# Performance work log

Hardware: AMD Instinct MI355X
Metric: run time of the kernel (lower is better)

The kernel has to match this reference:

```python
import jax, jax.numpy as jnp
import numpy as np

B = 4096
NQ = 4  # qubits -> 16-dim state vector


def _make_ops(seed, n_ops):
    # Deterministic stand-in for tq.RandomLayer: random RX/RY/RZ/CRX gates.
    rng = np.random.default_rng(seed)
    ops = []
    for _ in range(n_ops):
        kind = int(rng.integers(0, 4))
        if kind == 3:  # CRX on two distinct wires
            w = rng.choice(NQ, size=2, replace=False)
            ops.append((3, int(w[0]), int(w[1])))
        else:
            ops.append((kind, int(rng.integers(0, NQ)), 0))
    return ops

ENC_OPS = _make_ops(1, 8)    # QuantumPatchEncoder.random_layer (n_ops=8)
QFC_OPS = _make_ops(2, 50)   # QuantumFullyConnectedLayer.random_layer (n_ops=50)

_H = np.array([[1, 1], [1, -1]], np.complex64) * np.complex64(1.0 / np.sqrt(2.0))
_SX = np.array([[1 + 1j, 1 - 1j], [1 - 1j, 1 + 1j]], np.complex64) * np.complex64(0.5)
_CNOT = np.array([[1, 0, 0, 0], [0, 1, 0, 0], [0, 0, 0, 1], [0, 0, 1, 0]], np.complex64)


def _rx(t):
    c = jnp.cos(t / 2) + 0j
    s = -1j * jnp.sin(t / 2)
    return jnp.stack([jnp.stack([c, s], -1), jnp.stack([s, c], -1)], -2)


def _ry(t):
    c = jnp.cos(t / 2) + 0j
    s = jnp.sin(t / 2) + 0j
    return jnp.stack([jnp.stack([c, -s], -1), jnp.stack([s, c], -1)], -2)


def _rz(t):
    e0 = jnp.exp(-1j * t / 2)
    e1 = jnp.exp(1j * t / 2)
    z = jnp.zeros_like(e0)
    return jnp.stack([jnp.stack([e0, z], -1), jnp.stack([z, e1], -1)], -2)


def _crx(t):
    return jnp.eye(4, dtype=jnp.complex64).at[2:, 2:].set(_rx(t))


def _apply1(state, U, w):
    # state: (B, 2,2,2,2); U: (2,2) or per-sample (B,2,2)
    state = jnp.moveaxis(state, w + 1, -1)
    if U.ndim == 3:
        state = jnp.einsum('b...i,bji->b...j', state, U)
    else:
        state = jnp.einsum('...i,ji->...j', state, U)
    return jnp.moveaxis(state, -1, w + 1)


def _apply2(state, U, w0, w1):
    state = jnp.moveaxis(state, (w0 + 1, w1 + 1), (-2, -1))
    shp = state.shape
    state = state.reshape(shp[:-2] + (4,)) @ U.T
    return jnp.moveaxis(state.reshape(shp), (-2, -1), (w0 + 1, w1 + 1))


def _random_layer(state, ops, params):
    for i, (kind, w0, w1) in enumerate(ops):
        t = params[i]
        if kind == 0:
            state = _apply1(state, _rx(t), w0)
        elif kind == 1:
            state = _apply1(state, _ry(t), w0)
        elif kind == 2:
            state = _apply1(state, _rz(t), w0)
        else:
            state = _apply2(state, _crx(t), w0, w1)
    return state


def _measure_z(state):
    # <Z> on each wire from |amp|^2 marginals
    probs = state.real ** 2 + state.imag ** 2
    exps = []
    for w in range(NQ):
        axes = tuple(a for a in range(1, NQ + 1) if a != w + 1)
        m = probs.sum(axes)  # (B, 2)
        exps.append(m[:, 0] - m[:, 1])
    return jnp.stack(exps, 1)


def _conv(x, W, b):
    y = jax.lax.conv_general_dilated(x, W, (1, 1), 'SAME',
                                     dimension_numbers=('NCHW', 'OIHW', 'NCHW'))
    return y + b[None, :, None, None]


def _pool(x):
    return jax.lax.reduce_window(x, -jnp.inf, jax.lax.max,
                                 (1, 1, 2, 2), (1, 1, 2, 2), 'VALID')


def setup_inputs() -> dict:
    key = jax.random.key(0)
    ks = jax.random.split(key, 8)
    f = lambda k, shp, fan: jax.random.normal(k, shp, jnp.float32) / np.float32(np.sqrt(fan))
    two_pi = float(2 * np.pi)
    return {
        'x': jax.random.uniform(ks[0], (B, 1, 32, 32), jnp.float32),
        'conv1_w': f(ks[1], (8, 1, 3, 3), 9),
        'conv1_b': jnp.zeros((8,), jnp.float32),
        'conv2_w': f(ks[2], (16, 8, 3, 3), 72),
        'conv2_b': jnp.zeros((16,), jnp.float32),
        'enc_params': jax.random.uniform(ks[3], (8,), jnp.float32, 0.0, two_pi),
        'qfc_rand_params': jax.random.uniform(ks[4], (50,), jnp.float32, 0.0, two_pi),
        'qfc_params': jax.random.uniform(ks[5], (4,), jnp.float32, 0.0, two_pi),
        'bn_gamma': jnp.ones((4,), jnp.float32),
        'bn_beta': jnp.zeros((4,), jnp.float32),
        'fc_w': f(ks[6], (10, 68), 68),
        'fc_b': jnp.zeros((10,), jnp.float32),
    }


def reference(x, conv1_w, conv1_b, conv2_w, conv2_b, enc_params, qfc_rand_params,
              qfc_params, bn_gamma, bn_beta, fc_w, fc_b):
    # CNN feature extractor
    h = _pool(jax.nn.relu(_conv(x, conv1_w, conv1_b)))
    h = _pool(jax.nn.relu(_conv(h, conv2_w, conv2_b)))  # (B, 16, 8, 8)
    b = h.shape[0]
    pm = h.mean(1)  # channel-mean, (B, 8, 8)
    # 2x2 patches, row-major within patch, scanning r then c -> (B, 16, 4)
    patches = pm.reshape(b, 4, 2, 4, 2).transpose(0, 1, 3, 2, 4).reshape(b, 16, 4)

    # Encoder: fresh |0000> per patch (GeneralEncoder resets state); batch all
    # B*16 patch circuits together instead of looping.
    data = patches.reshape(b * 16, 4)
    state = jnp.zeros((b * 16, 16), jnp.complex64).at[:, 0].set(1.0)
    state = state.reshape(b * 16, 2, 2, 2, 2)
    for w in range(NQ):
        state = _apply1(state, _ry(data[:, w]), w)
    state = _random_layer(state, ENC_OPS, enc_params)
    qfeat = _measure_z(state).reshape(b, 64)  # (B, 16*4)

    # QFC operates on the state left by the LAST patch (as in the original)
    s = state.reshape(b, 16, 2, 2, 2, 2)[:, 15]
    s = _random_layer(s, QFC_OPS, qfc_rand_params)
    s = _apply1(s, _rx(qfc_params[0]), 0)
    s = _apply1(s, _ry(qfc_params[1]), 1)
    s = _apply1(s, _rz(qfc_params[2]), 3)
    s = _apply2(s, _crx(qfc_params[3]), 0, 2)
    s = _apply1(s, jnp.asarray(_H), 3)
    s = _apply1(s, jnp.asarray(_SX), 2)
    s = _apply2(s, jnp.asarray(_CNOT), 3, 0)
    q = _measure_z(s)  # (B, 4)

    # BatchNorm1d(4), training-mode (batch stats, biased var)
    mu = q.mean(0)
    var = q.var(0)
    q = (q - mu) / jnp.sqrt(var + 1e-5) * bn_gamma + bn_beta

    feats = jnp.concatenate([qfeat, q], 1)  # (B, 68)
    logits = feats @ fc_w.T + fc_b
    return jax.nn.log_softmax(logits, -1)
```

## Files before the change

kernel.cpp:

```cpp
#include <hip/hip_runtime.h>
#include <cstdint>

namespace crng {

typedef unsigned __int128 u128;

struct PCG {
    u128 state, inc;
    bool has32;
    uint32_t buf32;
};

constexpr u128 PCG_MULT = (((u128)2549297995355413924ULL) << 64) | (u128)4865540595714422341ULL;

constexpr uint64_t pcg_next64(PCG& g) {
    g.state = g.state * PCG_MULT + g.inc;
    uint64_t hi = (uint64_t)(g.state >> 64), lo = (uint64_t)g.state;
    unsigned rot = (unsigned)(g.state >> 122) & 63u;
    uint64_t v = hi ^ lo;
    return (v >> rot) | (v << ((64u - rot) & 63u));
}

constexpr uint32_t pcg_next32(PCG& g) {
    if (g.has32) { g.has32 = false; return g.buf32; }
    uint64_t n = pcg_next64(g);
    g.has32 = true;
    g.buf32 = (uint32_t)(n >> 32);
    return (uint32_t)n;
}

constexpr uint32_t hashmix(uint32_t& hc, uint32_t v) {
    v ^= hc; hc *= 0x931e8875u; v *= hc; v ^= v >> 16; return v;
}
constexpr uint32_t mixf(uint32_t x, uint32_t y) {
    uint32_t r = 0xca01f9ddu * x - 0x4973f715u * y;
    r ^= r >> 16;
    return r;
}

constexpr PCG seed_pcg(uint32_t entropy) {
    uint32_t pool[4] = {0, 0, 0, 0};
    uint32_t hc = 0x43b0d7e5u;
    pool[0] = hashmix(hc, entropy);
    for (int i = 1; i < 4; ++i) pool[i] = hashmix(hc, 0u);
    for (int s = 0; s < 4; ++s)
        for (int d = 0; d < 4; ++d)
            if (s != d) pool[d] = mixf(pool[d], hashmix(hc, pool[s]));

    uint32_t hb = 0x8b51f9ddu;
    uint32_t w[8] = {0, 0, 0, 0, 0, 0, 0, 0};
    for (int i = 0; i < 8; ++i) {
        uint32_t dv = pool[i & 3];
        dv ^= hb; hb *= 0x58f38dedu; dv *= hb; dv ^= dv >> 16;
        w[i] = dv;
    }
    uint64_t w64[4] = {0, 0, 0, 0};
    for (int i = 0; i < 4; ++i)
        w64[i] = (uint64_t)w[2 * i] | ((uint64_t)w[2 * i + 1] << 32);

    u128 initstate = (((u128)w64[0]) << 64) | (u128)w64[1];
    u128 initseq   = (((u128)w64[2]) << 64) | (u128)w64[3];
    PCG g = {};
    g.state = 0;
    g.inc = (initseq << 1) | (u128)1;
    g.state = g.state * PCG_MULT + g.inc;
    g.state += initstate;
    g.state = g.state * PCG_MULT + g.inc;
    g.has32 = false;
    g.buf32 = 0;
    return g;
}

constexpr uint32_t lemire32(PCG& g, uint32_t rng) {
    uint64_t rng_excl = (uint64_t)rng + 1;
    uint64_t m = (uint64_t)pcg_next32(g) * rng_excl;
    uint32_t leftover = (uint32_t)m;
    if (leftover < (uint32_t)rng_excl) {
        uint32_t threshold = (uint32_t)((uint64_t)(0xFFFFFFFFu - rng) % rng_excl);
        while (leftover < threshold) {
            m = (uint64_t)pcg_next32(g) * rng_excl;
            leftover = (uint32_t)m;
        }
    }
    return (uint32_t)(m >> 32);
}

struct Ops {
    int enc[8];
    int qfc[50];
};

constexpr void fill_ops(PCG& g, int n, int* out) {
    for (int i = 0; i < n; ++i) {
        uint32_t kind = lemire32(g, 3);
        uint32_t w0 = 0, w1 = 0;
        if (kind == 3) {
            uint32_t v2 = lemire32(g, 2);
            uint32_t v3 = lemire32(g, 3);
            uint32_t a0 = v2;
            uint32_t a1 = (v3 == v2) ? 3u : v3;
            uint32_t j = lemire32(g, 1);
            if (j == 0) { uint32_t t = a0; a0 = a1; a1 = t; }
            w0 = a0; w1 = a1;
        } else {
            w0 = lemire32(g, 3);
        }
        out[i] = (int)((kind << 4) | (w0 << 2) | w1);
    }
}

constexpr Ops make_ops_ct() {
    Ops o = {};
    PCG g1 = seed_pcg(1u);
    fill_ops(g1, 8, o.enc);
    PCG g2 = seed_pcg(2u);
    fill_ops(g2, 50, o.qfc);
    return o;
}

}

constexpr crng::Ops kOps = crng::make_ops_ct();

typedef _Float16 half8 __attribute__((ext_vector_type(8)));
typedef float float4v __attribute__((ext_vector_type(4)));

#define XS_STRIDE 24
#define XS_PLANE  (34 * XS_STRIDE)
#define XS_TOT    (2 * XS_PLANE)
#define H1F_ROW   (18 * 8)

__global__ __launch_bounds__(256, 4) void cnn_kernel(
    const float* __restrict__ x, const float* __restrict__ w1,
    const float* __restrict__ b1, const float* __restrict__ w2,
    const float* __restrict__ b2, float* __restrict__ pm,
    float* __restrict__ stats)
{
    __shared__ float xs[XS_TOT];
    __shared__ __align__(16) _Float16 h1f[18 * H1F_ROW];
    __shared__ __align__(16) _Float16 Ahalf[9 * 16 * 8];
    __shared__ float w1s[72], b1s[8], b2s[16];

    const int tid = threadIdx.x;
    const int b = blockIdx.x;
    const float* xb = x + (size_t)b * 1024;

    for (int k = tid; k < XS_TOT; k += 256) xs[k] = 0.f;
    for (int k = tid; k < 18 * H1F_ROW; k += 256) h1f[k] = (_Float16)0.f;
    for (int e = tid; e < 1152; e += 256) {
        int uv = e >> 7, m = (e >> 3) & 15, ci = e & 7;
        Ahalf[e] = (_Float16)w2[m * 72 + ci * 9 + uv];
    }
    if (tid < 72) w1s[tid] = w1[tid];
    if (tid < 8) b1s[tid] = b1[tid];
    if (tid < 16) b2s[tid] = b2[tid];
    if (b == 0 && tid < 8) stats[tid] = 0.f;
    __syncthreads();

    for (int k = tid; k < 1024; k += 256) {
        int r = k >> 5, c = k & 31;
        int p = c & 1;
        int q = p ? ((c + 1) >> 1) : (c >> 1);
        xs[p * XS_PLANE + (r + 1) * XS_STRIDE + q] = xb[k];
    }
    __syncthreads();

    {
        const int i = tid >> 4, j = tid & 15;
        float patch[4][4];
#pragma unroll
        for (int u = 0; u < 4; ++u) {
            int r = 2 * i + u;
            const float* ev = &xs[r * XS_STRIDE + j];
            const float* od = &xs[XS_PLANE + r * XS_STRIDE + j];
            patch[u][0] = od[0];
            patch[u][1] = ev[0];
            patch[u][2] = od[1];
            patch[u][3] = ev[1];
        }
        half8 hv;
#pragma unroll
        for (int c = 0; c < 8; ++c) {
            float m = -3.4e38f;
#pragma unroll
            for (int di = 0; di < 2; ++di)
#pragma unroll
                for (int dj = 0; dj < 2; ++dj) {
                    float acc = b1s[c];
#pragma unroll
                    for (int u = 0; u < 3; ++u)
#pragma unroll
                        for (int v = 0; v < 3; ++v)
                            acc += w1s[c * 9 + u * 3 + v] * patch[di + u][dj + v];
                    m = fmaxf(m, acc);
                }
            hv[c] = (_Float16)fmaxf(m, 0.f);
        }
        *(half8*)&h1f[(i + 1) * H1F_ROW + (j + 1) * 8] = hv;
    }
    __syncthreads();

    {
        const int w = tid >> 6;
        const int lane = tid & 63;
        const int pj = lane & 15;
        const int quad = lane >> 4;

        half8 afrag[9];
#pragma unroll
        for (int uv = 0; uv < 9; ++uv) {
            half8 a = {};
            if (quad == 0) a = *(const half8*)&Ahalf[(uv * 16 + pj) * 8];
            afrag[uv] = a;
        }

        float4v acc[4];
#pragma unroll
        for (int tl = 0; tl < 4; ++tl) {
            float4v c;
#pragma unroll
            for (int r = 0; r < 4; ++r) c[r] = b2s[4 * quad + r];
            acc[tl] = c;
        }

#pragma unroll
        for (int tl = 0; tl < 4; ++tl) {
            const int t = 4 * w + tl;
#pragma unroll
            for (int u = 0; u < 3; ++u) {
#pragma unroll
                for (int v = 0; v < 3; ++v) {
                    half8 bf = *(const half8*)&h1f[(t + u) * H1F_ROW + (pj + v) * 8];
                    acc[tl] = __builtin_amdgcn_mfma_f32_16x16x32_f16(
                        afrag[u * 3 + v], bf, acc[tl], 0, 0, 0);
                }
            }
        }

#pragma unroll
        for (int p = 0; p < 2; ++p) {
            float4v m1;
#pragma unroll
            for (int r = 0; r < 4; ++r)
                m1[r] = fmaxf(acc[2 * p][r], acc[2 * p + 1][r]);
            float s = 0.f;
#pragma unroll
            for (int r = 0; r < 4; ++r) {
                float o = __shfl_xor((float)m1[r], 1, 64);
                float mv = fmaxf(fmaxf(m1[r], o), 0.f);
                s += mv;
            }
            s += __shfl_xor(s, 16, 64);
            s += __shfl_xor(s, 32, 64);
            if (quad == 0 && !(pj & 1)) {
                const int i2 = 2 * w + p, j2 = pj >> 1;
                pm[(size_t)b * 64 + i2 * 8 + j2] = s * (1.f / 16.f);
            }
        }
    }
}

template<int KIND, int W0, int W1>
__device__ __forceinline__ void gate_ct(float (&ur)[16], float (&ui)[16],
                                        float ch, float sh)
{
    constexpr bool CTRL = (KIND == 3 || KIND == 6);
    constexpr int STT = CTRL ? (8 >> W1) : (8 >> W0);
    constexpr int STC = CTRL ? (8 >> W0) : 0;
#pragma unroll
    for (int k0 = 0; k0 < 16; ++k0) {
        if (k0 & STT) continue;
        if (STC != 0 && !(k0 & STC)) continue;
        const int k1 = k0 | STT;
        float x0r = ur[k0], x0i = ui[k0], x1r = ur[k1], x1i = ui[k1];
        if constexpr (KIND == 0 || KIND == 3) {
            ur[k0] = ch * x0r + sh * x1i;  ui[k0] = ch * x0i - sh * x1r;
            ur[k1] = sh * x0i + ch * x1r;  ui[k1] = -sh * x0r + ch * x1i;
        } else if constexpr (KIND == 1) {
            ur[k0] = ch * x0r - sh * x1r;  ui[k0] = ch * x0i - sh * x1i;
            ur[k1] = sh * x0r + ch * x1r;  ui[k1] = sh * x0i + ch * x1i;
        } else if constexpr (KIND == 2) {
            ur[k0] = ch * x0r + sh * x0i;  ui[k0] = ch * x0i - sh * x0r;
            ur[k1] = ch * x1r - sh * x1i;  ui[k1] = ch * x1i + sh * x1r;
        } else if constexpr (KIND == 4) {
            constexpr float RH = 0.70710678118654752f;
            ur[k0] = RH * (x0r + x1r);  ui[k0] = RH * (x0i + x1i);
            ur[k1] = RH * (x0r - x1r);  ui[k1] = RH * (x0i - x1i);
        } else if constexpr (KIND == 5) {
            ur[k0] = 0.5f * (x0r + x1r) - 0.5f * x0i + 0.5f * x1i;
            ui[k0] = 0.5f * (x0i + x1i) + 0.5f * x0r - 0.5f * x1r;
            ur[k1] = 0.5f * (x0r + x1r) + 0.5f * x0i - 0.5f * x1i;
            ui[k1] = 0.5f * (x0i + x1i) - 0.5f * x0r + 0.5f * x1r;
        } else {
            ur[k0] = x1r; ui[k0] = x1i;
            ur[k1] = x0r; ui[k1] = x0i;
        }
    }
}

template<int I>
__device__ __forceinline__ void run_enc(float (&ur)[16], float (&ui)[16],
                                        const float* ch, const float* sh)
{
    if constexpr (I < 8) {
        constexpr int op = kOps.enc[I];
        gate_ct<(op >> 4) & 7, (op >> 2) & 3, op & 3>(ur, ui, ch[I], sh[I]);
        run_enc<I + 1>(ur, ui, ch, sh);
    }
}

template<int I>
__device__ __forceinline__ void run_qfc(float (&ur)[16], float (&ui)[16],
                                        const float* ch, const float* sh)
{
    if constexpr (I < 50) {
        constexpr int op = kOps.qfc[I];
        gate_ct<(op >> 4) & 7, (op >> 2) & 3, op & 3>(ur, ui, ch[I], sh[I]);
        run_qfc<I + 1>(ur, ui, ch, sh);
    }
}

__global__ __launch_bounds__(256) void quantum_kernel(
    const float* __restrict__ pm, const float* __restrict__ encp,
    const float* __restrict__ qfcr, const float* __restrict__ qfcp,
    float* __restrict__ qfeat, float* __restrict__ qraw,
    float* __restrict__ stats, int Bv)
{
    __shared__ float chs[62], shs[62];
    __shared__ float rstat[128];

    const int tid = threadIdx.x;
    if (tid < 62) {
        float t = (tid < 8) ? encp[tid] : (tid < 58) ? qfcr[tid - 8] : qfcp[tid - 58];
        chs[tid] = cosf(0.5f * t);
        shs[tid] = sinf(0.5f * t);
    }
    __syncthreads();

    const int gid = blockIdx.x * 256 + tid;
    const int b = gid >> 4, p = gid & 15;
    float qq[4] = {0.f, 0.f, 0.f, 0.f};
    bool last = false;

    if (b < Bv) {
        const int pr = p >> 2, pc = p & 3;
        const float* pmb = pm + (size_t)b * 64;
        float d0 = pmb[(2 * pr) * 8 + 2 * pc];
        float d1 = pmb[(2 * pr) * 8 + 2 * pc + 1];
        float d2 = pmb[(2 * pr + 1) * 8 + 2 * pc];
        float d3 = pmb[(2 * pr + 1) * 8 + 2 * pc + 1];
        float f0c = cosf(0.5f * d0), f0s = sinf(0.5f * d0);
        float f1c = cosf(0.5f * d1), f1s = sinf(0.5f * d1);
        float f2c = cosf(0.5f * d2), f2s = sinf(0.5f * d2);
        float f3c = cosf(0.5f * d3), f3s = sinf(0.5f * d3);

        float ur[16], ui[16];
#pragma unroll
        for (int k = 0; k < 16; ++k) {
            float v = ((k & 8) ? f0s : f0c);
            v *= ((k & 4) ? f1s : f1c);
            v *= ((k & 2) ? f2s : f2c);
            v *= ((k & 1) ? f3s : f3c);
            ur[k] = v;
            ui[k] = 0.f;
        }
        run_enc<0>(ur, ui, chs, shs);

        float qv[4] = {0.f, 0.f, 0.f, 0.f};
#pragma unroll
        for (int k = 0; k < 16; ++k) {
            float pk = ur[k] * ur[k] + ui[k] * ui[k];
            qv[0] += (k & 8) ? -pk : pk;
            qv[1] += (k & 4) ? -pk : pk;
            qv[2] += (k & 2) ? -pk : pk;
            qv[3] += (k & 1) ? -pk : pk;
        }
        *(float4*)(qfeat + (size_t)b * 64 + p * 4) = make_float4(qv[0], qv[1], qv[2], qv[3]);

        if (p == 15) {
            last = true;
            run_qfc<0>(ur, ui, chs + 8, shs + 8);
            gate_ct<0, 0, 0>(ur, ui, chs[58], shs[58]);
            gate_ct<1, 1, 0>(ur, ui, chs[59], shs[59]);
            gate_ct<2, 3, 0>(ur, ui, chs[60], shs[60]);
            gate_ct<3, 0, 2>(ur, ui, chs[61], shs[61]);
            gate_ct<4, 3, 0>(ur, ui, 0.f, 0.f);
            gate_ct<5, 2, 0>(ur, ui, 0.f, 0.f);
            gate_ct<6, 3, 0>(ur, ui, 0.f, 0.f);
#pragma unroll
            for (int k = 0; k < 16; ++k) {
                float pk = ur[k] * ur[k] + ui[k] * ui[k];
                qq[0] += (k & 8) ? -pk : pk;
                qq[1] += (k & 4) ? -pk : pk;
                qq[2] += (k & 2) ? -pk : pk;
                qq[3] += (k & 1) ? -pk : pk;
            }
            *(float4*)(qraw + (size_t)b * 4) = make_float4(qq[0], qq[1], qq[2], qq[3]);
        }
    }

    for (int k = tid; k < 128; k += 256) rstat[k] = 0.f;
    __syncthreads();
    const int m = tid >> 4;
    if (last) {
#pragma unroll
        for (int w = 0; w < 4; ++w) {
            rstat[w * 16 + m] = qq[w];
            rstat[64 + w * 16 + m] = qq[w] * qq[w];
        }
    }
    __syncthreads();
    if (tid < 8) {
        float s = 0.f;
#pragma unroll
        for (int k = 0; k < 16; ++k) s += rstat[tid * 16 + k];
        atomicAdd(&stats[tid], s);
    }
}

__global__ __launch_bounds__(256) void head_kernel(
    const float* __restrict__ qfeat, const float* __restrict__ qraw,
    const float* __restrict__ stats, const float* __restrict__ gam,
    const float* __restrict__ bet, const float* __restrict__ fcw,
    const float* __restrict__ fcb, float* __restrict__ out, int Bv)
{
    __shared__ float Wf[680];
    __shared__ float bf[10], st[8], ga[4], be[4];
    const int tid = threadIdx.x;
    for (int k = tid; k < 680; k += 256) Wf[k] = fcw[k];
    if (tid < 10) bf[tid] = fcb[tid];
    if (tid < 8) st[tid] = stats[tid];
    if (tid < 4) { ga[tid] = gam[tid]; be[tid] = bet[tid]; }
    __syncthreads();

    const int b = blockIdx.x * 256 + tid;
    if (b >= Bv) return;

    const float invB = 1.f / (float)Bv;

    float logit[10];
#pragma unroll
    for (int k = 0; k < 10; ++k) logit[k] = bf[k];

    const float* qf = qfeat + (size_t)b * 64;
    for (int j = 0; j < 64; ++j) {
        float v = qf[j];
#pragma unroll
        for (int k = 0; k < 10; ++k) logit[k] += v * Wf[k * 68 + j];
    }
    float4 qr = *(const float4*)(qraw + (size_t)b * 4);
    float qn[4] = {qr.x, qr.y, qr.z, qr.w};
#pragma unroll
    for (int w = 0; w < 4; ++w) {
        float mu = st[w] * invB;
        float var = st[4 + w] * invB - mu * mu;
        float v = (qn[w] - mu) / sqrtf(var + 1e-5f) * ga[w] + be[w];
#pragma unroll
        for (int k = 0; k < 10; ++k) logit[k] += v * Wf[k * 68 + 64 + w];
    }

    float m = logit[0];
#pragma unroll
    for (int k = 1; k < 10; ++k) m = fmaxf(m, logit[k]);
    float sum = 0.f;
#pragma unroll
    for (int k = 0; k < 10; ++k) sum += expf(logit[k] - m);
    float lse = logf(sum);
#pragma unroll
    for (int k = 0; k < 10; ++k) out[(size_t)b * 10 + k] = logit[k] - m - lse;
}

extern "C" void kernel_launch(void* const* d_in, const int* in_sizes, int n_in,
                              void* d_out, int out_size, void* d_ws, size_t ws_size,
                              hipStream_t stream)
{
    const float* x    = (const float*)d_in[0];
    const float* w1   = (const float*)d_in[1];
    const float* b1   = (const float*)d_in[2];
    const float* w2   = (const float*)d_in[3];
    const float* b2   = (const float*)d_in[4];
    const float* encp = (const float*)d_in[5];
    const float* qfcr = (const float*)d_in[6];
    const float* qfcp = (const float*)d_in[7];
    const float* gam  = (const float*)d_in[8];
    const float* bet  = (const float*)d_in[9];
    const float* fcw  = (const float*)d_in[10];
    const float* fcb  = (const float*)d_in[11];
    float* out = (float*)d_out;

    const int Bv = in_sizes[0] / 1024;

    float* pm    = (float*)d_ws;
    float* qfeat = pm + (size_t)Bv * 64;
    float* qraw  = qfeat + (size_t)Bv * 64;
    float* stats = qraw + (size_t)Bv * 4;

    cnn_kernel<<<Bv, 256, 0, stream>>>(x, w1, b1, w2, b2, pm, stats);
    quantum_kernel<<<(Bv * 16 + 255) / 256, 256, 0, stream>>>(
        pm, encp, qfcr, qfcp, qfeat, qraw, stats, Bv);
    head_kernel<<<(Bv + 255) / 256, 256, 0, stream>>>(qfeat, qraw, stats, gam, bet,
                                                      fcw, fcb, out, Bv);
}
```

Measured before the change: 140.4 us.

## Fuse CNN with encoder and QFC with head using grid barrier

Runs the patch encoder inside the CNN kernel on pooled features kept in LDS, so the pm buffer and the separate quantum kernel go away. The QFC circuit, BatchNorm statistics and the FC/log-softmax head now share one tail kernel, with a software grid barrier on an atomic counter between the stats reduction and the normalisation. Also vectorises the input load and qfeat reads and replaces the LDS stat reduction with wave shuffles. This removes one launch and some global round trips. The spin barrier assumes all 16 tail blocks are co-resident, and the encoder now runs on only 16 of 256 threads per block.

Result: faster. 129.6 us (-7.7%).

```diff
diff --git a/kernel.cpp b/kernel.cpp
--- a/kernel.cpp
+++ b/kernel.cpp
@@ -129,136 +129,6 @@
 #define XS_PLANE  (34 * XS_STRIDE)
 #define XS_TOT    (2 * XS_PLANE)
 #define H1F_ROW   (18 * 8)
-
-__global__ __launch_bounds__(256, 4) void cnn_kernel(
-    const float* __restrict__ x, const float* __restrict__ w1,
-    const float* __restrict__ b1, const float* __restrict__ w2,
-    const float* __restrict__ b2, float* __restrict__ pm,
-    float* __restrict__ stats)
-{
-    __shared__ float xs[XS_TOT];
-    __shared__ __align__(16) _Float16 h1f[18 * H1F_ROW];
-    __shared__ __align__(16) _Float16 Ahalf[9 * 16 * 8];
-    __shared__ float w1s[72], b1s[8], b2s[16];
-
-    const int tid = threadIdx.x;
-    const int b = blockIdx.x;
-    const float* xb = x + (size_t)b * 1024;
-
-    for (int k = tid; k < XS_TOT; k += 256) xs[k] = 0.f;
-    for (int k = tid; k < 18 * H1F_ROW; k += 256) h1f[k] = (_Float16)0.f;
-    for (int e = tid; e < 1152; e += 256) {
-        int uv = e >> 7, m = (e >> 3) & 15, ci = e & 7;
-        Ahalf[e] = (_Float16)w2[m * 72 + ci * 9 + uv];
-    }
-    if (tid < 72) w1s[tid] = w1[tid];
-    if (tid < 8) b1s[tid] = b1[tid];
-    if (tid < 16) b2s[tid] = b2[tid];
-    if (b == 0 && tid < 8) stats[tid] = 0.f;
-    __syncthreads();
-
-    for (int k = tid; k < 1024; k += 256) {
-        int r = k >> 5, c = k & 31;
-        int p = c & 1;
-        int q = p ? ((c + 1) >> 1) : (c >> 1);
-        xs[p * XS_PLANE + (r + 1) * XS_STRIDE + q] = xb[k];
-    }
-    __syncthreads();
-
-    {
-        const int i = tid >> 4, j = tid & 15;
-        float patch[4][4];
-#pragma unroll
-        for (int u = 0; u < 4; ++u) {
-            int r = 2 * i + u;
-            const float* ev = &xs[r * XS_STRIDE + j];
-            const float* od = &xs[XS_PLANE + r * XS_STRIDE + j];
-            patch[u][0] = od[0];
-            patch[u][1] = ev[0];
-            patch[u][2] = od[1];
-            patch[u][3] = ev[1];
-        }
-        half8 hv;
-#pragma unroll
-        for (int c = 0; c < 8; ++c) {
-            float m = -3.4e38f;
-#pragma unroll
-            for (int di = 0; di < 2; ++di)
-#pragma unroll
-                for (int dj = 0; dj < 2; ++dj) {
-                    float acc = b1s[c];
-#pragma unroll
-                    for (int u = 0; u < 3; ++u)
-#pragma unroll
-                        for (int v = 0; v < 3; ++v)
-                            acc += w1s[c * 9 + u * 3 + v] * patch[di + u][dj + v];
-                    m = fmaxf(m, acc);
-                }
-            hv[c] = (_Float16)fmaxf(m, 0.f);
-        }
-        *(half8*)&h1f[(i + 1) * H1F_ROW + (j + 1) * 8] = hv;
-    }
-    __syncthreads();
-
-    {
-        const int w = tid >> 6;
-        const int lane = tid & 63;
-        const int pj = lane & 15;
-        const int quad = lane >> 4;
-
-        half8 afrag[9];
-#pragma unroll
-        for (int uv = 0; uv < 9; ++uv) {
-            half8 a = {};
-            if (quad == 0) a = *(const half8*)&Ahalf[(uv * 16 + pj) * 8];
-            afrag[uv] = a;
-        }
-
-        float4v acc[4];
-#pragma unroll
-        for (int tl = 0; tl < 4; ++tl) {
-            float4v c;
-#pragma unroll
-            for (int r = 0; r < 4; ++r) c[r] = b2s[4 * quad + r];
-            acc[tl] = c;
-        }
-
-#pragma unroll
-        for (int tl = 0; tl < 4; ++tl) {
-            const int t = 4 * w + tl;
-#pragma unroll
-            for (int u = 0; u < 3; ++u) {
-#pragma unroll
-                for (int v = 0; v < 3; ++v) {
-                    half8 bf = *(const half8*)&h1f[(t + u) * H1F_ROW + (pj + v) * 8];
-                    acc[tl] = __builtin_amdgcn_mfma_f32_16x16x32_f16(
-                        afrag[u * 3 + v], bf, acc[tl], 0, 0, 0);
-                }
-            }
-        }
-
-#pragma unroll
-        for (int p = 0; p < 2; ++p) {
-            float4v m1;
-#pragma unroll
-            for (int r = 0; r < 4; ++r)
-                m1[r] = fmaxf(acc[2 * p][r], acc[2 * p + 1][r]);
-            float s = 0.f;
-#pragma unroll
-            for (int r = 0; r < 4; ++r) {
-                float o = __shfl_xor((float)m1[r], 1, 64);
-                float mv = fmaxf(fmaxf(m1[r], o), 0.f);
-                s += mv;
-            }
-            s += __shfl_xor(s, 16, 64);
-            s += __shfl_xor(s, 32, 64);
-            if (quad == 0 && !(pj & 1)) {
-                const int i2 = 2 * w + p, j2 = pj >> 1;
-                pm[(size_t)b * 64 + i2 * 8 + j2] = s * (1.f / 16.f);
-            }
-        }
-    }
-}
 
 template<int KIND, int W0, int W1>
 __device__ __forceinline__ void gate_ct(float (&ur)[16], float (&ui)[16],
@@ -320,35 +190,155 @@
     }
 }
 
-__global__ __launch_bounds__(256) void quantum_kernel(
-    const float* __restrict__ pm, const float* __restrict__ encp,
-    const float* __restrict__ qfcr, const float* __restrict__ qfcp,
-    float* __restrict__ qfeat, float* __restrict__ qraw,
-    float* __restrict__ stats, int Bv)
+__global__ __launch_bounds__(256, 4) void cnn_enc_kernel(
+    const float* __restrict__ x, const float* __restrict__ w1,
+    const float* __restrict__ b1, const float* __restrict__ w2,
+    const float* __restrict__ b2, const float* __restrict__ encp,
+    float* __restrict__ qfeat, float* __restrict__ sstate,
+    float* __restrict__ stats, int* __restrict__ bar)
 {
-    __shared__ float chs[62], shs[62];
-    __shared__ float rstat[128];
+    __shared__ float xs[XS_TOT];
+    __shared__ __align__(16) _Float16 h1f[18 * H1F_ROW];
+    __shared__ __align__(16) _Float16 Ahalf[9 * 16 * 8];
+    __shared__ float w1s[72], b1s[8], b2s[16];
+    __shared__ float pm_lds[64];
+    __shared__ float chsE[8], shsE[8];
 
     const int tid = threadIdx.x;
-    if (tid < 62) {
-        float t = (tid < 8) ? encp[tid] : (tid < 58) ? qfcr[tid - 8] : qfcp[tid - 58];
-        chs[tid] = cosf(0.5f * t);
-        shs[tid] = sinf(0.5f * t);
-    }
-    __syncthreads();
-
-    const int gid = blockIdx.x * 256 + tid;
-    const int b = gid >> 4, p = gid & 15;
-    float qq[4] = {0.f, 0.f, 0.f, 0.f};
-    bool last = false;
-
-    if (b < Bv) {
-        const int pr = p >> 2, pc = p & 3;
-        const float* pmb = pm + (size_t)b * 64;
-        float d0 = pmb[(2 * pr) * 8 + 2 * pc];
-        float d1 = pmb[(2 * pr) * 8 + 2 * pc + 1];
-        float d2 = pmb[(2 * pr + 1) * 8 + 2 * pc];
-        float d3 = pmb[(2 * pr + 1) * 8 + 2 * pc + 1];
+    const int b = blockIdx.x;
+    const float* xb = x + (size_t)b * 1024;
+
+    for (int k = tid; k < XS_TOT; k += 256) xs[k] = 0.f;
+    for (int k = tid; k < 18 * H1F_ROW; k += 256) h1f[k] = (_Float16)0.f;
+    for (int e = tid; e < 1152; e += 256) {
+        int uv = e >> 7, m = (e >> 3) & 15, ci = e & 7;
+        Ahalf[e] = (_Float16)w2[m * 72 + ci * 9 + uv];
+    }
+    if (tid < 72) w1s[tid] = w1[tid];
+    if (tid < 8) b1s[tid] = b1[tid];
+    if (tid < 16) b2s[tid] = b2[tid];
+    if (tid < 8) {
+        float t = encp[tid];
+        chsE[tid] = cosf(0.5f * t);
+        shsE[tid] = sinf(0.5f * t);
+    }
+    if (b == 0 && tid < 8) stats[tid] = 0.f;
+    if (b == 0 && tid == 8) *bar = 0;
+    __syncthreads();
+
+    {
+        const int r = tid >> 3, m = tid & 7;
+        float4 v = *(const float4*)(xb + (size_t)tid * 4);
+        float* d0p = &xs[(r + 1) * XS_STRIDE + 2 * m];
+        float* d1p = &xs[XS_PLANE + (r + 1) * XS_STRIDE + 2 * m];
+        d0p[0] = v.x;
+        d1p[1] = v.y;
+        d0p[1] = v.z;
+        d1p[2] = v.w;
+    }
+    __syncthreads();
+
+    {
+        const int i = tid >> 4, j = tid & 15;
+        float patch[4][4];
+#pragma unroll
+        for (int u = 0; u < 4; ++u) {
+            int r = 2 * i + u;
+            const float* ev = &xs[r * XS_STRIDE + j];
+            const float* od = &xs[XS_PLANE + r * XS_STRIDE + j];
+            patch[u][0] = od[0];
+            patch[u][1] = ev[0];
+            patch[u][2] = od[1];
+            patch[u][3] = ev[1];
+        }
+        half8 hv;
+#pragma unroll
+        for (int c = 0; c < 8; ++c) {
+            float m = -3.4e38f;
+#pragma unroll
+            for (int di = 0; di < 2; ++di)
+#pragma unroll
+                for (int dj = 0; dj < 2; ++dj) {
+                    float acc = b1s[c];
+#pragma unroll
+                    for (int u = 0; u < 3; ++u)
+#pragma unroll
+                        for (int v = 0; v < 3; ++v)
+                            acc += w1s[c * 9 + u * 3 + v] * patch[di + u][dj + v];
+                    m = fmaxf(m, acc);
+                }
+            hv[c] = (_Float16)fmaxf(m, 0.f);
+        }
+        *(half8*)&h1f[(i + 1) * H1F_ROW + (j + 1) * 8] = hv;
+    }
+    __syncthreads();
+
+    {
+        const int w = tid >> 6;
+        const int lane = tid & 63;
+        const int pj = lane & 15;
+        const int quad = lane >> 4;
+
+        half8 afrag[9];
+#pragma unroll
+        for (int uv = 0; uv < 9; ++uv) {
+            half8 a = {};
+            if (quad == 0) a = *(const half8*)&Ahalf[(uv * 16 + pj) * 8];
+            afrag[uv] = a;
+        }
+
+        float4v acc[4];
+#pragma unroll
+        for (int tl = 0; tl < 4; ++tl) {
+            float4v c;
+#pragma unroll
+            for (int r = 0; r < 4; ++r) c[r] = b2s[4 * quad + r];
+            acc[tl] = c;
+        }
+
+#pragma unroll
+        for (int tl = 0; tl < 4; ++tl) {
+            const int t = 4 * w + tl;
+#pragma unroll
+            for (int u = 0; u < 3; ++u) {
+#pragma unroll
+                for (int v = 0; v < 3; ++v) {
+                    half8 bf = *(const half8*)&h1f[(t + u) * H1F_ROW + (pj + v) * 8];
+                    acc[tl] = __builtin_amdgcn_mfma_f32_16x16x32_f16(
+                        afrag[u * 3 + v], bf, acc[tl], 0, 0, 0);
+                }
+            }
+        }
+
+#pragma unroll
+        for (int p = 0; p < 2; ++p) {
+            float4v m1;
+#pragma unroll
+            for (int r = 0; r < 4; ++r)
+                m1[r] = fmaxf(acc[2 * p][r], acc[2 * p + 1][r]);
+            float s = 0.f;
+#pragma unroll
+            for (int r = 0; r < 4; ++r) {
+                float o = __shfl_xor((float)m1[r], 1, 64);
+                float mv = fmaxf(fmaxf(m1[r], o), 0.f);
+                s += mv;
+            }
+            s += __shfl_xor(s, 16, 64);
+            s += __shfl_xor(s, 32, 64);
+            if (quad == 0 && !(pj & 1)) {
+                const int i2 = 2 * w + p, j2 = pj >> 1;
+                pm_lds[i2 * 8 + j2] = s * (1.f / 16.f);
+            }
+        }
+    }
+    __syncthreads();
+
+    if (tid < 16) {
+        const int p = tid, pr = p >> 2, pc = p & 3;
+        float d0 = pm_lds[(2 * pr) * 8 + 2 * pc];
+        float d1 = pm_lds[(2 * pr) * 8 + 2 * pc + 1];
+        float d2 = pm_lds[(2 * pr + 1) * 8 + 2 * pc];
+        float d3 = pm_lds[(2 * pr + 1) * 8 + 2 * pc + 1];
         float f0c = cosf(0.5f * d0), f0s = sinf(0.5f * d0);
         float f1c = cosf(0.5f * d1), f1s = sinf(0.5f * d1);
         float f2c = cosf(0.5f * d2), f2s = sinf(0.5f * d2);
@@ -364,7 +354,7 @@
             ur[k] = v;
             ui[k] = 0.f;
         }
-        run_enc<0>(ur, ui, chs, shs);
+        run_enc<0>(ur, ui, chsE, shsE);
 
         float qv[4] = {0.f, 0.f, 0.f, 0.f};
 #pragma unroll
@@ -375,86 +365,135 @@
             qv[2] += (k & 2) ? -pk : pk;
             qv[3] += (k & 1) ? -pk : pk;
         }
-        *(float4*)(qfeat + (size_t)b * 64 + p * 4) = make_float4(qv[0], qv[1], qv[2], qv[3]);
+        *(float4*)(qfeat + (size_t)b * 64 + p * 4) =
+            make_float4(qv[0], qv[1], qv[2], qv[3]);
 
         if (p == 15) {
-            last = true;
-            run_qfc<0>(ur, ui, chs + 8, shs + 8);
-            gate_ct<0, 0, 0>(ur, ui, chs[58], shs[58]);
-            gate_ct<1, 1, 0>(ur, ui, chs[59], shs[59]);
-            gate_ct<2, 3, 0>(ur, ui, chs[60], shs[60]);
-            gate_ct<3, 0, 2>(ur, ui, chs[61], shs[61]);
-            gate_ct<4, 3, 0>(ur, ui, 0.f, 0.f);
-            gate_ct<5, 2, 0>(ur, ui, 0.f, 0.f);
-            gate_ct<6, 3, 0>(ur, ui, 0.f, 0.f);
-#pragma unroll
-            for (int k = 0; k < 16; ++k) {
-                float pk = ur[k] * ur[k] + ui[k] * ui[k];
-                qq[0] += (k & 8) ? -pk : pk;
-                qq[1] += (k & 4) ? -pk : pk;
-                qq[2] += (k & 2) ? -pk : pk;
-                qq[3] += (k & 1) ? -pk : pk;
-            }
-            *(float4*)(qraw + (size_t)b * 4) = make_float4(qq[0], qq[1], qq[2], qq[3]);
-        }
-    }
-
-    for (int k = tid; k < 128; k += 256) rstat[k] = 0.f;
-    __syncthreads();
-    const int m = tid >> 4;
-    if (last) {
-#pragma unroll
-        for (int w = 0; w < 4; ++w) {
-            rstat[w * 16 + m] = qq[w];
-            rstat[64 + w * 16 + m] = qq[w] * qq[w];
-        }
-    }
-    __syncthreads();
-    if (tid < 8) {
-        float s = 0.f;
-#pragma unroll
-        for (int k = 0; k < 16; ++k) s += rstat[tid * 16 + k];
-        atomicAdd(&stats[tid], s);
-    }
-}
-
-__global__ __launch_bounds__(256) void head_kernel(
-    const float* __restrict__ qfeat, const float* __restrict__ qraw,
-    const float* __restrict__ stats, const float* __restrict__ gam,
-    const float* __restrict__ bet, const float* __restrict__ fcw,
-    const float* __restrict__ fcb, float* __restrict__ out, int Bv)
+            float4* sp = (float4*)(sstate + (size_t)b * 32);
+#pragma unroll
+            for (int i = 0; i < 4; ++i)
+                sp[i] = make_float4(ur[4 * i], ur[4 * i + 1], ur[4 * i + 2], ur[4 * i + 3]);
+#pragma unroll
+            for (int i = 0; i < 4; ++i)
+                sp[4 + i] = make_float4(ui[4 * i], ui[4 * i + 1], ui[4 * i + 2], ui[4 * i + 3]);
+        }
+    }
+}
+
+__global__ __launch_bounds__(256) void tail_kernel(
+    const float* __restrict__ sstate, const float* __restrict__ qfeat,
+    const float* __restrict__ qfcr, const float* __restrict__ qfcp,
+    const float* __restrict__ gam, const float* __restrict__ bet,
+    const float* __restrict__ fcw, const float* __restrict__ fcb,
+    float* __restrict__ stats, int* __restrict__ bar,
+    float* __restrict__ out, int Bv, int NBlk)
 {
+    __shared__ float chs[54], shs[54];
     __shared__ float Wf[680];
-    __shared__ float bf[10], st[8], ga[4], be[4];
+    __shared__ float bfs[10], st8[8], ga[4], be[4];
+    __shared__ float rstat[32];
+
     const int tid = threadIdx.x;
+    if (tid < 54) {
+        float t = (tid < 50) ? qfcr[tid] : qfcp[tid - 50];
+        chs[tid] = cosf(0.5f * t);
+        shs[tid] = sinf(0.5f * t);
+    }
     for (int k = tid; k < 680; k += 256) Wf[k] = fcw[k];
-    if (tid < 10) bf[tid] = fcb[tid];
-    if (tid < 8) st[tid] = stats[tid];
+    if (tid < 10) bfs[tid] = fcb[tid];
     if (tid < 4) { ga[tid] = gam[tid]; be[tid] = bet[tid]; }
     __syncthreads();
 
     const int b = blockIdx.x * 256 + tid;
+    float qq[4] = {0.f, 0.f, 0.f, 0.f};
+
+    if (b < Bv) {
+        float ur[16], ui[16];
+        const float4* sp = (const float4*)(sstate + (size_t)b * 32);
+#pragma unroll
+        for (int i = 0; i < 4; ++i) {
+            float4 v = sp[i];
+            ur[4 * i] = v.x; ur[4 * i + 1] = v.y; ur[4 * i + 2] = v.z; ur[4 * i + 3] = v.w;
+        }
+#pragma unroll
+        for (int i = 0; i < 4; ++i) {
+            float4 v = sp[4 + i];
+            ui[4 * i] = v.x; ui[4 * i + 1] = v.y; ui[4 * i + 2] = v.z; ui[4 * i + 3] = v.w;
+        }
+
+        run_qfc<0>(ur, ui, chs, shs);
+        gate_ct<0, 0, 0>(ur, ui, chs[50], shs[50]);
+        gate_ct<1, 1, 0>(ur, ui, chs[51], shs[51]);
+        gate_ct<2, 3, 0>(ur, ui, chs[52], shs[52]);
+        gate_ct<3, 0, 2>(ur, ui, chs[53], shs[53]);
+        gate_ct<4, 3, 0>(ur, ui, 0.f, 0.f);
+        gate_ct<5, 2, 0>(ur, ui, 0.f, 0.f);
+        gate_ct<6, 3, 0>(ur, ui, 0.f, 0.f);
+
+#pragma unroll
+        for (int k = 0; k < 16; ++k) {
+            float pk = ur[k] * ur[k] + ui[k] * ui[k];
+            qq[0] += (k & 8) ? -pk : pk;
+            qq[1] += (k & 4) ? -pk : pk;
+            qq[2] += (k & 2) ? -pk : pk;
+            qq[3] += (k & 1) ? -pk : pk;
+        }
+    }
+
+    {
+        const int lane = tid & 63, wv = tid >> 6;
+#pragma unroll
+        for (int q = 0; q < 8; ++q) {
+            float v = (q < 4) ? qq[q] : qq[q - 4] * qq[q - 4];
+            v += __shfl_xor(v, 1, 64);
+            v += __shfl_xor(v, 2, 64);
+            v += __shfl_xor(v, 4, 64);
+            v += __shfl_xor(v, 8, 64);
+            v += __shfl_xor(v, 16, 64);
+            v += __shfl_xor(v, 32, 64);
+            if (lane == 0) rstat[q * 4 + wv] = v;
+        }
+        __syncthreads();
+        if (tid < 8)
+            atomicAdd(&stats[tid], rstat[tid * 4] + rstat[tid * 4 + 1] +
+                                   rstat[tid * 4 + 2] + rstat[tid * 4 + 3]);
+    }
+
+    __syncthreads();
+    if (tid == 0) {
+        __threadfence();
+        atomicAdd(bar, 1);
+        while (atomicAdd(bar, 0) < NBlk)
+            __builtin_amdgcn_s_sleep(8);
+    }
+    __syncthreads();
+
+    if (tid < 8) st8[tid] = atomicAdd(&stats[tid], 0.f);
+    __syncthreads();
+
     if (b >= Bv) return;
 
     const float invB = 1.f / (float)Bv;
 
     float logit[10];
 #pragma unroll
-    for (int k = 0; k < 10; ++k) logit[k] = bf[k];
+    for (int k = 0; k < 10; ++k) logit[k] = bfs[k];
 
     const float* qf = qfeat + (size_t)b * 64;
-    for (int j = 0; j < 64; ++j) {
-        float v = qf[j];
-#pragma unroll
-        for (int k = 0; k < 10; ++k) logit[k] += v * Wf[k * 68 + j];
-    }
-    float4 qr = *(const float4*)(qraw + (size_t)b * 4);
-    float qn[4] = {qr.x, qr.y, qr.z, qr.w};
+#pragma unroll
+    for (int j4 = 0; j4 < 16; ++j4) {
+        float4 v = *(const float4*)(qf + 4 * j4);
+#pragma unroll
+        for (int k = 0; k < 10; ++k) {
+            const float* wr = &Wf[k * 68 + 4 * j4];
+            logit[k] += v.x * wr[0] + v.y * wr[1] + v.z * wr[2] + v.w * wr[3];
+        }
+    }
 #pragma unroll
     for (int w = 0; w < 4; ++w) {
-        float mu = st[w] * invB;
-        float var = st[4 + w] * invB - mu * mu;
-        float v = (qn[w] - mu) / sqrtf(var + 1e-5f) * ga[w] + be[w];
+        float mu = st8[w] * invB;
+        float var = st8[4 + w] * invB - mu * mu;
+        float v = (qq[w] - mu) / sqrtf(var + 1e-5f) * ga[w] + be[w];
 #pragma unroll
         for (int k = 0; k < 10; ++k) logit[k] += v * Wf[k * 68 + 64 + w];
     }
@@ -490,14 +529,15 @@
 
     const int Bv = in_sizes[0] / 1024;
 
-    float* pm    = (float*)d_ws;
-    float* qfeat = pm + (size_t)Bv * 64;
-    float* qraw  = qfeat + (size_t)Bv * 64;
-    float* stats = qraw + (size_t)Bv * 4;
-
-    cnn_kernel<<<Bv, 256, 0, stream>>>(x, w1, b1, w2, b2, pm, stats);
-    quantum_kernel<<<(Bv * 16 + 255) / 256, 256, 0, stream>>>(
-        pm, encp, qfcr, qfcp, qfeat, qraw, stats, Bv);
-    head_kernel<<<(Bv + 255) / 256, 256, 0, stream>>>(qfeat, qraw, stats, gam, bet,
-                                                      fcw, fcb, out, Bv);
-}
+    float* qfeat  = (float*)d_ws;
+    float* sstate = qfeat + (size_t)Bv * 64;
+    float* stats  = sstate + (size_t)Bv * 32;
+    int*   bar    = (int*)(stats + 8);
+
+    cnn_enc_kernel<<<Bv, 256, 0, stream>>>(x, w1, b1, w2, b2, encp,
+                                           qfeat, sstate, stats, bar);
+
+    const int nblk = (Bv + 255) / 256;
+    tail_kernel<<<nblk, 256, 0, stream>>>(sstate, qfeat, qfcr, qfcp, gam, bet,
+                                          fcw, fcb, stats, bar, out, Bv, nblk);
+}
```
